# Optimization experiments

Measured on AMD Instinct MI355X. Metric: run time of the kernel, lower is better.

The kernel has to match this reference:

```python
import jax, jax.numpy as jnp
import numpy as np

EPS = 1e-6


def setup_inputs() -> dict:
    key = jax.random.key(0)
    kq, kk, kv = jax.random.split(key, 3)
    B, H, S, D = 4, 16, 4096, 64
    Q = jax.random.normal(kq, (B, H, S, D), dtype=jnp.float32)
    K = jax.random.normal(kk, (B, H, S, D), dtype=jnp.float32)
    V = jax.random.normal(kv, (B, H, S, D), dtype=jnp.float32)
    mask = jnp.ones((B, S), dtype=bool)
    return {"Q": Q, "K": K, "V": V, "mask": mask}


def reference(Q, K, V, mask):
    # Feature map: relu(sinh(x)), applied to Q and K
    Qf = jax.nn.relu(jnp.sinh(Q))            # [B,H,S,D]
    Kf = jax.nn.relu(jnp.sinh(K))            # [B,H,S,D]
    # Zero out padded key positions: mask is [B,S]
    Kf = Kf * mask[:, None, :, None].astype(Kf.dtype)
    # K^T V outer product over sequence: [B,H,D,D]
    attn_inter = jnp.einsum('bhsd,bhse->bhde', Kf, V)
    # Q (K^T V): [B,H,S,D]
    attn_weights = jnp.einsum('bhqd,bhde->bhqe', Qf, attn_inter)
    # Normalizer: Q . sum_s |K_masked| (Kf is nonneg after relu, abs kept for fidelity)
    k_sum = jnp.abs(Kf).sum(axis=2)          # [B,H,D]
    norm = jnp.einsum('bhqd,bhd->bhq', Qf, k_sum)[..., None]  # [B,H,S,1]
    norm = jnp.maximum(norm, EPS)
    return attn_weights / norm
```

## Files before the change

### kernel.cpp

```cpp
#include <hip/hip_runtime.h>
#include <hip/hip_bf16.h>
#include <cstdint>

#define SEQ  4096
#define DIM  64
#define NBH  64
#define FEPS 1e-6f
#define MSTRIDE 4160

typedef __attribute__((ext_vector_type(8))) short bf16x8;
typedef __attribute__((ext_vector_type(4))) float f32x4;

__device__ __forceinline__ float featmap(float x) {
    return x > 0.0f ? 0.5f * (__expf(x) - __expf(-x)) : 0.0f;
}

__device__ __forceinline__ unsigned short f2bf(float x) {
    unsigned int u = __float_as_uint(x);
    u += 0x7fffu + ((u >> 16) & 1u);
    return (unsigned short)(u >> 16);
}

__global__ __launch_bounds__(256, 4) void k_phase1(
    const float* __restrict__ K, const float* __restrict__ V,
    const int* __restrict__ mask, float* __restrict__ partM,
    int nchunk, int rows_per_chunk)
{
    const int chunk = blockIdx.x;
    const int bh    = blockIdx.y;
    const int b     = bh >> 4;
    const int tid   = threadIdx.x;
    const int wave  = tid >> 6;
    const int lane  = tid & 63;
    const int ty    = lane >> 3;
    const int tx    = lane & 7;

    __shared__ __align__(16) float lds[8704];
    float* ldsK = lds;
    float* ldsV = lds + 4352;

    const float* Kb = K + (size_t)bh * SEQ * DIM;
    const float* Vb = V + (size_t)bh * SEQ * DIM;
    const int*   mb = mask + (size_t)b * SEQ;

    float acc[8][8];
    #pragma unroll
    for (int i = 0; i < 8; ++i)
        #pragma unroll
        for (int j = 0; j < 8; ++j) acc[i][j] = 0.0f;
    float ks[8];
    #pragma unroll
    for (int i = 0; i < 8; ++i) ks[i] = 0.0f;

    const int srow = tid >> 2;
    const int sc   = tid & 3;
    const int nstage = rows_per_chunk >> 6;

    for (int stage = 0; stage < nstage; ++stage) {
        const int sb = chunk * rows_per_chunk + stage * 64;
        const int mrow = mb[sb + srow];
        const float4* krow = (const float4*)(Kb + (size_t)(sb + srow) * DIM);
        const float4* vrow = (const float4*)(Vb + (size_t)(sb + srow) * DIM);
        #pragma unroll
        for (int i = 0; i < 4; ++i) {
            float4 kq = krow[sc * 4 + i];
            float4 vq = vrow[sc * 4 + i];
            float4 kf;
            kf.x = mrow ? featmap(kq.x) : 0.0f;
            kf.y = mrow ? featmap(kq.y) : 0.0f;
            kf.z = mrow ? featmap(kq.z) : 0.0f;
            kf.w = mrow ? featmap(kq.w) : 0.0f;
            *(float4*)&ldsK[srow * 68 + sc * 16 + 4 * i] = kf;
            *(float4*)&ldsV[srow * 68 + sc * 16 + 4 * i] = vq;
        }
        __syncthreads();
        for (int si = 0; si < 16; ++si) {
            const int s = si * 4 + wave;
            const float4 k0 = *(const float4*)&ldsK[s * 68 + ty * 8];
            const float4 k1 = *(const float4*)&ldsK[s * 68 + ty * 8 + 4];
            const float4 v0 = *(const float4*)&ldsV[s * 68 + tx * 8];
            const float4 v1 = *(const float4*)&ldsV[s * 68 + tx * 8 + 4];
            const float kf[8] = {k0.x,k0.y,k0.z,k0.w,k1.x,k1.y,k1.z,k1.w};
            const float vv[8] = {v0.x,v0.y,v0.z,v0.w,v1.x,v1.y,v1.z,v1.w};
            #pragma unroll
            for (int i = 0; i < 8; ++i) {
                ks[i] += kf[i];
                #pragma unroll
                for (int j = 0; j < 8; ++j)
                    acc[i][j] = fmaf(kf[i], vv[j], acc[i][j]);
            }
        }
        __syncthreads();
    }

    if (wave < 2) {
        float* rd = lds + wave * 4096;
        #pragma unroll
        for (int i = 0; i < 8; ++i) {
            *(float4*)&rd[(ty*8+i)*64 + tx*8]     = make_float4(acc[i][0],acc[i][1],acc[i][2],acc[i][3]);
            *(float4*)&rd[(ty*8+i)*64 + tx*8 + 4] = make_float4(acc[i][4],acc[i][5],acc[i][6],acc[i][7]);
        }
        if (tx == 0) {
            float* kr = lds + 8192 + wave * 64;
            #pragma unroll
            for (int i = 0; i < 8; ++i) kr[ty*8+i] = ks[i];
        }
    }
    __syncthreads();
    if (wave >= 2) {
        float* rd = lds + (wave - 2) * 4096;
        #pragma unroll
        for (int i = 0; i < 8; ++i)
            #pragma unroll
            for (int j = 0; j < 8; ++j)
                rd[(ty*8+i)*64 + tx*8 + j] += acc[i][j];
        if (tx == 0) {
            float* kr = lds + 8192 + (wave - 2) * 64;
            #pragma unroll
            for (int i = 0; i < 8; ++i) kr[ty*8+i] += ks[i];
        }
    }
    __syncthreads();

    float* dst = partM + (size_t)(bh * nchunk + chunk) * MSTRIDE;
    float4* dst4 = (float4*)dst;
    const float4* q0 = (const float4*)lds;
    const float4* q1 = (const float4*)(lds + 4096);
    #pragma unroll
    for (int t = 0; t < 4; ++t) {
        const int j = tid + t * 256;
        float4 a = q0[j], c = q1[j];
        dst4[j] = make_float4(a.x+c.x, a.y+c.y, a.z+c.z, a.w+c.w);
    }
    if (tid < 64) dst[4096 + tid] = lds[8192 + tid] + lds[8256 + tid];
}

__global__ __launch_bounds__(256) void k_reduce(
    const float* __restrict__ partM, float* __restrict__ finalM, int nchunk)
{
    const int bh  = blockIdx.x;
    const int tid = threadIdx.x;
    const float4* src = (const float4*)(partM + (size_t)bh * nchunk * MSTRIDE);
    float4* dst = (float4*)(finalM + (size_t)bh * MSTRIDE);
    for (int q = tid; q < MSTRIDE / 4; q += 256) {
        float4 s = src[q];
        for (int c = 1; c < nchunk; ++c) {
            float4 t = src[(size_t)c * (MSTRIDE / 4) + q];
            s.x += t.x; s.y += t.y; s.z += t.z; s.w += t.w;
        }
        dst[q] = s;
    }
}

__global__ __launch_bounds__(256, 4) void k_phase2(
    const float* __restrict__ Q, const float* __restrict__ finalM,
    float* __restrict__ out)
{
    const int bh   = blockIdx.y;
    const int tid  = threadIdx.x;
    const int wave = tid >> 6;
    const int lane = tid & 63;
    const int r    = lane & 15;
    const int g    = lane >> 4;

    const float* Mb = finalM + (size_t)bh * MSTRIDE;

    bf16x8 bfr[4][2];
    float  ksl[2][8];
    #pragma unroll
    for (int kk = 0; kk < 2; ++kk)
        #pragma unroll
        for (int j = 0; j < 8; ++j) {
            const int d = kk*32 + g*8 + j;
            ksl[kk][j] = Mb[4096 + d];
            #pragma unroll
            for (int nt = 0; nt < 4; ++nt)
                bfr[nt][kk][j] = (short)f2bf(Mb[d*64 + nt*16 + r]);
        }

    const int q0 = blockIdx.x * 64 + wave * 16;
    const float* Qrow = Q + (size_t)bh * SEQ * DIM + (size_t)(q0 + r) * DIM;

    bf16x8 afr[2];
    float z = 0.0f;
    #pragma unroll
    for (int kk = 0; kk < 2; ++kk) {
        float4 x0 = *(const float4*)(Qrow + kk*32 + g*8);
        float4 x1 = *(const float4*)(Qrow + kk*32 + g*8 + 4);
        const float qf[8] = {featmap(x0.x), featmap(x0.y), featmap(x0.z), featmap(x0.w),
                             featmap(x1.x), featmap(x1.y), featmap(x1.z), featmap(x1.w)};
        #pragma unroll
        for (int j = 0; j < 8; ++j) {
            z = fmaf(qf[j], ksl[kk][j], z);
            afr[kk][j] = (short)f2bf(qf[j]);
        }
    }
    z += __shfl_xor(z, 16);
    z += __shfl_xor(z, 32);

    f32x4 acc[4];
    #pragma unroll
    for (int nt = 0; nt < 4; ++nt) acc[nt] = (f32x4){0.f, 0.f, 0.f, 0.f};
    #pragma unroll
    for (int kk = 0; kk < 2; ++kk)
        #pragma unroll
        for (int nt = 0; nt < 4; ++nt)
            acc[nt] = __builtin_amdgcn_mfma_f32_16x16x32_bf16(
                afr[kk], bfr[nt][kk], acc[nt], 0, 0, 0);

    float rinv[4];
    #pragma unroll
    for (int j = 0; j < 4; ++j) {
        const float zc = __shfl(z, g*4 + j);
        rinv[j] = 1.0f / fmaxf(zc, FEPS);
    }
    float* Ob = out + (size_t)bh * SEQ * DIM;
    #pragma unroll
    for (int nt = 0; nt < 4; ++nt)
        #pragma unroll
        for (int j = 0; j < 4; ++j)
            Ob[(size_t)(q0 + g*4 + j) * DIM + nt*16 + r] = acc[nt][j] * rinv[j];
}

extern "C" void kernel_launch(void* const* d_in, const int* in_sizes, int n_in,
                              void* d_out, int out_size, void* d_ws, size_t ws_size,
                              hipStream_t stream) {
    const float* Q    = (const float*)d_in[0];
    const float* K    = (const float*)d_in[1];
    const float* V    = (const float*)d_in[2];
    const int*   mask = (const int*)d_in[3];
    float* out = (float*)d_out;
    float* ws  = (float*)d_ws;

    int nchunk = 16;
    while (nchunk > 1 &&
           ws_size < (size_t)(NBH * nchunk + NBH) * MSTRIDE * sizeof(float))
        nchunk >>= 1;
    const int rows = SEQ / nchunk;

    float* partM  = ws;
    float* finalM = ws + (size_t)NBH * nchunk * MSTRIDE;

    k_phase1<<<dim3(nchunk, NBH), 256, 0, stream>>>(K, V, mask, partM, nchunk, rows);
    k_reduce<<<NBH, 256, 0, stream>>>(partM, finalM, nchunk);
    k_phase2<<<dim3(64, NBH), 256, 0, stream>>>(Q, finalM, out);
}
```

Measured before the change: 269.9 us.

## Compute K^T V partial sums with bf16 MFMA and split reduce across blocks

Phase 1 drops the LDS-staged fp32 outer-product accumulation. Each wave now loads K and V directly from global memory, applies the feature map, converts to bf16 and accumulates its 16-row slice of K^T V with 16x16x32 MFMA instructions. This removes the LDS traffic, the barriers and the cross-wave reduction. The reduce kernel is also split four ways per head to expose more parallelism. In exchange, the K^T V accumulation now uses bf16 inputs, which lowers precision, and the strided scalar global loads may coalesce poorly.

```diff
diff --git a/kernel.cpp b/kernel.cpp
--- a/kernel.cpp
+++ b/kernel.cpp
@@ -15,10 +15,10 @@
     return x > 0.0f ? 0.5f * (__expf(x) - __expf(-x)) : 0.0f;
 }
 
-__device__ __forceinline__ unsigned short f2bf(float x) {
+__device__ __forceinline__ short f2bf(float x) {
     unsigned int u = __float_as_uint(x);
     u += 0x7fffu + ((u >> 16) & 1u);
-    return (unsigned short)(u >> 16);
+    return (short)(u >> 16);
 }
 
 __global__ __launch_bounds__(256, 4) void k_phase1(
@@ -32,117 +32,70 @@
     const int tid   = threadIdx.x;
     const int wave  = tid >> 6;
     const int lane  = tid & 63;
-    const int ty    = lane >> 3;
-    const int tx    = lane & 7;
-
-    __shared__ __align__(16) float lds[8704];
-    float* ldsK = lds;
-    float* ldsV = lds + 4352;
+    const int r     = lane & 15;
+    const int g     = lane >> 4;
 
     const float* Kb = K + (size_t)bh * SEQ * DIM;
     const float* Vb = V + (size_t)bh * SEQ * DIM;
     const int*   mb = mask + (size_t)b * SEQ;
 
-    float acc[8][8];
-    #pragma unroll
-    for (int i = 0; i < 8; ++i)
-        #pragma unroll
-        for (int j = 0; j < 8; ++j) acc[i][j] = 0.0f;
-    float ks[8];
-    #pragma unroll
-    for (int i = 0; i < 8; ++i) ks[i] = 0.0f;
-
-    const int srow = tid >> 2;
-    const int sc   = tid & 3;
-    const int nstage = rows_per_chunk >> 6;
-
-    for (int stage = 0; stage < nstage; ++stage) {
-        const int sb = chunk * rows_per_chunk + stage * 64;
-        const int mrow = mb[sb + srow];
-        const float4* krow = (const float4*)(Kb + (size_t)(sb + srow) * DIM);
-        const float4* vrow = (const float4*)(Vb + (size_t)(sb + srow) * DIM);
-        #pragma unroll
-        for (int i = 0; i < 4; ++i) {
-            float4 kq = krow[sc * 4 + i];
-            float4 vq = vrow[sc * 4 + i];
-            float4 kf;
-            kf.x = mrow ? featmap(kq.x) : 0.0f;
-            kf.y = mrow ? featmap(kq.y) : 0.0f;
-            kf.z = mrow ? featmap(kq.z) : 0.0f;
-            kf.w = mrow ? featmap(kq.w) : 0.0f;
-            *(float4*)&ldsK[srow * 68 + sc * 16 + 4 * i] = kf;
-            *(float4*)&ldsV[srow * 68 + sc * 16 + 4 * i] = vq;
-        }
-        __syncthreads();
-        for (int si = 0; si < 16; ++si) {
-            const int s = si * 4 + wave;
-            const float4 k0 = *(const float4*)&ldsK[s * 68 + ty * 8];
-            const float4 k1 = *(const float4*)&ldsK[s * 68 + ty * 8 + 4];
-            const float4 v0 = *(const float4*)&ldsV[s * 68 + tx * 8];
-            const float4 v1 = *(const float4*)&ldsV[s * 68 + tx * 8 + 4];
-            const float kf[8] = {k0.x,k0.y,k0.z,k0.w,k1.x,k1.y,k1.z,k1.w};
-            const float vv[8] = {v0.x,v0.y,v0.z,v0.w,v1.x,v1.y,v1.z,v1.w};
+    f32x4 acc[4];
+    #pragma unroll
+    for (int nt = 0; nt < 4; ++nt) acc[nt] = (f32x4){0.f, 0.f, 0.f, 0.f};
+    float ksp = 0.0f;
+
+    const int s0  = chunk * rows_per_chunk;
+    const int nks = rows_per_chunk >> 5;
+
+    for (int ks = 0; ks < nks; ++ks) {
+        const int srow = s0 + ks * 32 + g * 8;
+        const float* ka = Kb + (size_t)srow * DIM + wave * 16 + r;
+        const float* va = Vb + (size_t)srow * DIM + r;
+        const int*   ma = mb + srow;
+
+        bf16x8 af;
+        #pragma unroll
+        for (int j = 0; j < 8; ++j) {
+            float kf = featmap(ka[(size_t)j * DIM]);
+            kf = ma[j] ? kf : 0.0f;
+            ksp += kf;
+            af[j] = f2bf(kf);
+        }
+
+        bf16x8 bf[4];
+        #pragma unroll
+        for (int j = 0; j < 8; ++j)
             #pragma unroll
-            for (int i = 0; i < 8; ++i) {
-                ks[i] += kf[i];
-                #pragma unroll
-                for (int j = 0; j < 8; ++j)
-                    acc[i][j] = fmaf(kf[i], vv[j], acc[i][j]);
-            }
-        }
-        __syncthreads();
-    }
-
-    if (wave < 2) {
-        float* rd = lds + wave * 4096;
-        #pragma unroll
-        for (int i = 0; i < 8; ++i) {
-            *(float4*)&rd[(ty*8+i)*64 + tx*8]     = make_float4(acc[i][0],acc[i][1],acc[i][2],acc[i][3]);
-            *(float4*)&rd[(ty*8+i)*64 + tx*8 + 4] = make_float4(acc[i][4],acc[i][5],acc[i][6],acc[i][7]);
-        }
-        if (tx == 0) {
-            float* kr = lds + 8192 + wave * 64;
-            #pragma unroll
-            for (int i = 0; i < 8; ++i) kr[ty*8+i] = ks[i];
-        }
-    }
-    __syncthreads();
-    if (wave >= 2) {
-        float* rd = lds + (wave - 2) * 4096;
-        #pragma unroll
-        for (int i = 0; i < 8; ++i)
-            #pragma unroll
-            for (int j = 0; j < 8; ++j)
-                rd[(ty*8+i)*64 + tx*8 + j] += acc[i][j];
-        if (tx == 0) {
-            float* kr = lds + 8192 + (wave - 2) * 64;
-            #pragma unroll
-            for (int i = 0; i < 8; ++i) kr[ty*8+i] += ks[i];
-        }
-    }
-    __syncthreads();
+            for (int nt = 0; nt < 4; ++nt)
+                bf[nt][j] = f2bf(va[(size_t)j * DIM + nt * 16]);
+
+        #pragma unroll
+        for (int nt = 0; nt < 4; ++nt)
+            acc[nt] = __builtin_amdgcn_mfma_f32_16x16x32_bf16(
+                af, bf[nt], acc[nt], 0, 0, 0);
+    }
 
     float* dst = partM + (size_t)(bh * nchunk + chunk) * MSTRIDE;
-    float4* dst4 = (float4*)dst;
-    const float4* q0 = (const float4*)lds;
-    const float4* q1 = (const float4*)(lds + 4096);
-    #pragma unroll
-    for (int t = 0; t < 4; ++t) {
-        const int j = tid + t * 256;
-        float4 a = q0[j], c = q1[j];
-        dst4[j] = make_float4(a.x+c.x, a.y+c.y, a.z+c.z, a.w+c.w);
-    }
-    if (tid < 64) dst[4096 + tid] = lds[8192 + tid] + lds[8256 + tid];
+    #pragma unroll
+    for (int nt = 0; nt < 4; ++nt)
+        #pragma unroll
+        for (int j = 0; j < 4; ++j)
+            dst[(wave * 16 + g * 4 + j) * 64 + nt * 16 + r] = acc[nt][j];
+
+    ksp += __shfl_xor(ksp, 16);
+    ksp += __shfl_xor(ksp, 32);
+    if (lane < 16) dst[4096 + wave * 16 + lane] = ksp;
 }
 
 __global__ __launch_bounds__(256) void k_reduce(
     const float* __restrict__ partM, float* __restrict__ finalM, int nchunk)
 {
-    const int bh  = blockIdx.x;
+    const int bh  = blockIdx.y;
     const int tid = threadIdx.x;
     const float4* src = (const float4*)(partM + (size_t)bh * nchunk * MSTRIDE);
     float4* dst = (float4*)(finalM + (size_t)bh * MSTRIDE);
-    for (int q = tid; q < MSTRIDE / 4; q += 256) {
+    const int qend = blockIdx.x * 260 + 260;
+    for (int q = blockIdx.x * 260 + tid; q < qend; q += 256) {
         float4 s = src[q];
         for (int c = 1; c < nchunk; ++c) {
             float4 t = src[(size_t)c * (MSTRIDE / 4) + q];
@@ -175,7 +128,7 @@
             ksl[kk][j] = Mb[4096 + d];
             #pragma unroll
             for (int nt = 0; nt < 4; ++nt)
-                bfr[nt][kk][j] = (short)f2bf(Mb[d*64 + nt*16 + r]);
+                bfr[nt][kk][j] = f2bf(Mb[d*64 + nt*16 + r]);
         }
 
     const int q0 = blockIdx.x * 64 + wave * 16;
@@ -192,7 +145,7 @@
         #pragma unroll
         for (int j = 0; j < 8; ++j) {
             z = fmaf(qf[j], ksl[kk][j], z);
-            afr[kk][j] = (short)f2bf(qf[j]);
+            afr[kk][j] = f2bf(qf[j]);
         }
     }
     z += __shfl_xor(z, 16);
@@ -242,6 +195,6 @@
     float* finalM = ws + (size_t)NBH * nchunk * MSTRIDE;
 
     k_phase1<<<dim3(nchunk, NBH), 256, 0, stream>>>(K, V, mask, partM, nchunk, rows);
-    k_reduce<<<NBH, 256, 0, stream>>>(partM, finalM, nchunk);
+    k_reduce<<<dim3(4, NBH), 256, 0, stream>>>(partM, finalM, nchunk);
     k_phase2<<<dim3(64, NBH), 256, 0, stream>>>(Q, finalM, out);
 }
```

Result: faster. 247.5 us (-8.3%).
